# Kernel optimization log

Hardware: AMD Instinct MI355X
Metric: run time of the kernel (lower is better)

The kernel has to match this reference:

```python
import jax, jax.numpy as jnp
import numpy as np


def setup_inputs() -> dict:
    key = jax.random.key(0)
    ks = jax.random.split(key, 7)
    B, IN, H = 4096, 2048, 2048
    initrange = 1.0 / np.sqrt(H)
    return {
        "x": jax.random.normal(ks[0], (B, IN), dtype=jnp.float32),
        "h_prev": jax.random.normal(ks[1], (B, H), dtype=jnp.float32),
        "c_prev": jax.random.normal(ks[2], (B, H), dtype=jnp.float32),
        "W_x": jax.random.uniform(ks[3], (4 * H, IN), minval=-initrange, maxval=initrange, dtype=jnp.float32),
        "b_x": jax.random.uniform(ks[4], (4 * H,), minval=-initrange, maxval=initrange, dtype=jnp.float32),
        "W_h": jax.random.uniform(ks[5], (4 * H, H), minval=-initrange, maxval=initrange, dtype=jnp.float32),
        "b_h": jax.random.uniform(ks[6], (4 * H,), minval=-initrange, maxval=initrange, dtype=jnp.float32),
    }


def reference(x, h_prev, c_prev, W_x, b_x, W_h, b_h):
    # gates = Linear_x(x) + Linear_h(h_prev), shape [B, 4H]
    gates = x @ W_x.T + b_x + h_prev @ W_h.T + b_h
    i, f, g, o = jnp.split(gates, 4, axis=1)  # chunk order in original: i, f, g, o
    i = jax.nn.sigmoid(i)
    f = jax.nn.sigmoid(f)
    g = jnp.tanh(g)
    o = jax.nn.sigmoid(o)
    c = f * c_prev + i * g
    h = o * jnp.tanh(c)
    return (h, c)
```

## Files before the change

### kernel.cpp

```cpp
#include <hip/hip_runtime.h>
#include <hip/hip_bf16.h>
#include <stdint.h>


#define M_DIM 4096
#define N_PACK 8192
#define K_DIM 4096
#define H_DIM 2048

typedef __attribute__((ext_vector_type(8))) short bf16x8;
typedef __attribute__((ext_vector_type(4))) float f32x4;
typedef __attribute__((ext_vector_type(8))) unsigned short ushortx8;

__device__ __forceinline__ unsigned short f2bf(float f) {
    union { float f; uint32_t u; } v; v.f = f;
    uint32_t u = v.u;
    uint32_t r = (u + 0x7FFFu + ((u >> 16) & 1u)) >> 16;
    return (unsigned short)r;
}

__device__ __forceinline__ float fsigmoid(float x) { return 1.0f / (1.0f + __expf(-x)); }
__device__ __forceinline__ float ftanh(float x) { return 2.0f * fsigmoid(2.0f * x) - 1.0f; }

__global__ __launch_bounds__(256) void pack_a(const float* __restrict__ x,
                                              const float* __restrict__ h,
                                              unsigned short* __restrict__ A) {
    int i = blockIdx.x * 256 + threadIdx.x;
    int e = i * 8;
    int row = e >> 12;
    int col = e & 4095;
    const float* src = (col < H_DIM) ? (x + (size_t)row * H_DIM + col)
                                     : (h + (size_t)row * H_DIM + (col - H_DIM));
    float4 f0 = ((const float4*)src)[0];
    float4 f1 = ((const float4*)src)[1];
    ushortx8 o;
    o[0] = f2bf(f0.x); o[1] = f2bf(f0.y); o[2] = f2bf(f0.z); o[3] = f2bf(f0.w);
    o[4] = f2bf(f1.x); o[5] = f2bf(f1.y); o[6] = f2bf(f1.z); o[7] = f2bf(f1.w);
    *(ushortx8*)(A + e) = o;
}

__global__ __launch_bounds__(256) void pack_w(const float* __restrict__ Wx,
                                              const float* __restrict__ Wh,
                                              unsigned short* __restrict__ W) {
    int i = blockIdx.x * 256 + threadIdx.x;
    int e = i * 8;
    int p = e >> 12;
    int k = e & 4095;
    int g  = (p >> 4) & 3;
    int j  = ((p >> 6) << 4) | (p & 15);
    int orig = g * H_DIM + j;
    const float* src = (k < H_DIM) ? (Wx + (size_t)orig * H_DIM + k)
                                   : (Wh + (size_t)orig * H_DIM + (k - H_DIM));
    float4 f0 = ((const float4*)src)[0];
    float4 f1 = ((const float4*)src)[1];
    ushortx8 o;
    o[0] = f2bf(f0.x); o[1] = f2bf(f0.y); o[2] = f2bf(f0.z); o[3] = f2bf(f0.w);
    o[4] = f2bf(f1.x); o[5] = f2bf(f1.y); o[6] = f2bf(f1.z); o[7] = f2bf(f1.w);
    *(ushortx8*)(W + (size_t)p * K_DIM + k) = o;
}

__device__ __forceinline__ void gload_lds16(const void* g, void* l) {
    __builtin_amdgcn_global_load_lds(
        (const __attribute__((address_space(1))) void*)g,
        (__attribute__((address_space(3))) void*)l, 16, 0, 0);
}

#define BAR() __builtin_amdgcn_s_barrier()
#define LGKM0() asm volatile("s_waitcnt lgkmcnt(0)" ::: "memory")
#define VMCNT2() asm volatile("s_waitcnt vmcnt(2)" ::: "memory")
#define VMCNT0() asm volatile("s_waitcnt vmcnt(0)" ::: "memory")

__global__ __launch_bounds__(512, 2) void lstm_gemm8(
        const unsigned short* __restrict__ A,
        const unsigned short* __restrict__ W,
        const float* __restrict__ bx, const float* __restrict__ bh,
        const float* __restrict__ c_prev, float* __restrict__ out) {
    __shared__ char lds[2][2][32768];

    const int tid  = threadIdx.x;
    const int wid  = tid >> 6;
    const int lane = tid & 63;
    const int wr   = wid >> 2;
    const int wc   = wid & 3;

    const int swz = (blockIdx.x & 7) * 64 + (blockIdx.x >> 3);
    const int bm  = swz & 15;
    const int bn  = swz >> 4;

    const char* Ab = (const char*)A + (size_t)(bm * 256) * (K_DIM * 2);
    const char* Wb = (const char*)W + (size_t)(bn * 256) * (K_DIM * 2);

    const int srow = tid >> 3;
    const int skb  = ((tid & 7) << 4) ^ ((srow & 7) << 4);

    auto stage_half = [&](int buf, int mat, int h, int kt) {
        const char* gb = mat ? Wb : Ab;
        #pragma unroll
        for (int qq = 0; qq < 2; ++qq) {
            int q = h * 2 + qq;
            const char* src = gb + (size_t)(q * 64 + srow) * (K_DIM * 2) + kt * 128 + skb;
            gload_lds16(src, &lds[buf][mat][q * 8192 + tid * 16]);
        }
    };

    f32x4 acc[8][4] = {};
    bf16x8 A0[4][2], A1[4][2], Bq[2][2];

    auto read_a = [&](int buf, int qm, bf16x8 (&ar)[4][2]) {
        #pragma unroll
        for (int mf = 0; mf < 4; ++mf) {
            int row = wr * 128 + (qm * 4 + mf) * 16 + (lane & 15);
            #pragma unroll
            for (int kk = 0; kk < 2; ++kk) {
                int cb = (kk * 64 + ((lane >> 4) << 4)) ^ ((row & 7) << 4);
                ar[mf][kk] = *(const bf16x8*)&lds[buf][0][row * 128 + cb];
            }
        }
    };
    auto read_b = [&](int buf, int qn) {
        #pragma unroll
        for (int nf = 0; nf < 2; ++nf) {
            int row = wc * 64 + (qn * 2 + nf) * 16 + (lane & 15);
            #pragma unroll
            for (int kk = 0; kk < 2; ++kk) {
                int cb = (kk * 64 + ((lane >> 4) << 4)) ^ ((row & 7) << 4);
                Bq[nf][kk] = *(const bf16x8*)&lds[buf][1][row * 128 + cb];
            }
        }
    };

#define MMA_Q(QM, QN, AR)                                                      \
    do {                                                                       \
        __builtin_amdgcn_s_setprio(1);                                         \
        _Pragma("unroll")                                                      \
        for (int mf = 0; mf < 4; ++mf) {                                       \
            _Pragma("unroll")                                                  \
            for (int nf = 0; nf < 2; ++nf) {                                   \
                _Pragma("unroll")                                              \
                for (int kk = 0; kk < 2; ++kk) {                               \
                    acc[(QM)*4+mf][(QN)*2+nf] =                                \
                        __builtin_amdgcn_mfma_f32_16x16x32_bf16(               \
                            AR[mf][kk], Bq[nf][kk],                            \
                            acc[(QM)*4+mf][(QN)*2+nf], 0, 0, 0);               \
                }                                                              \
            }                                                                  \
        }                                                                      \
        __builtin_amdgcn_s_setprio(0);                                         \
    } while (0)

    stage_half(0, 0, 0, 0); stage_half(0, 0, 1, 0);
    stage_half(0, 1, 0, 0); stage_half(0, 1, 1, 0);
    stage_half(1, 0, 0, 1);
    VMCNT2();
    BAR();

    for (int it = 0; it < 32; ++it) {
        const int t1   = 2 * it + 1;
        const bool last = (it == 31);

        read_a(0, 0, A0); read_b(0, 0);
        stage_half(1, 0, 1, t1);
        BAR(); LGKM0(); MMA_Q(0, 0, A0); BAR();

        read_a(0, 1, A1);
        stage_half(1, 1, 0, t1);
        BAR(); LGKM0(); MMA_Q(1, 0, A1); BAR();

        read_b(0, 1);
        stage_half(1, 1, 1, t1);
        BAR(); LGKM0(); MMA_Q(0, 1, A0); BAR();

        if (!last) { stage_half(0, 0, 0, t1 + 1); VMCNT2(); }
        else       { VMCNT0(); }
        BAR(); LGKM0(); MMA_Q(1, 1, A1); BAR();

        read_a(1, 0, A0); read_b(1, 0);
        if (!last) stage_half(0, 0, 1, t1 + 1);
        BAR(); LGKM0(); MMA_Q(0, 0, A0); BAR();

        read_a(1, 1, A1);
        if (!last) stage_half(0, 1, 0, t1 + 1);
        BAR(); LGKM0(); MMA_Q(1, 0, A1); BAR();

        read_b(1, 1);
        if (!last) stage_half(0, 1, 1, t1 + 1);
        BAR(); LGKM0(); MMA_Q(0, 1, A0); BAR();

        if (!last) { stage_half(1, 0, 0, t1 + 2); VMCNT2(); }
        else       { VMCNT0(); }
        BAR(); LGKM0(); MMA_Q(1, 1, A1); BAR();
    }

    const int jlo  = lane & 15;
    const int rgrp = lane >> 4;
    const int j    = (bn * 4 + wc) * 16 + jlo;

    const float bi  = bx[j]             + bh[j];
    const float bff = bx[H_DIM + j]     + bh[H_DIM + j];
    const float bg  = bx[2 * H_DIM + j] + bh[2 * H_DIM + j];
    const float bo  = bx[3 * H_DIM + j] + bh[3 * H_DIM + j];

    float* out_h = out;
    float* out_c = out + (size_t)M_DIM * H_DIM;

    #pragma unroll
    for (int m = 0; m < 8; ++m) {
        int row0 = bm * 256 + wr * 128 + m * 16 + rgrp * 4;
        #pragma unroll
        for (int r = 0; r < 4; ++r) {
            int row = row0 + r;
            float pi = acc[m][0][r] + bi;
            float pf = acc[m][1][r] + bff;
            float pg = acc[m][2][r] + bg;
            float po = acc[m][3][r] + bo;
            float i_ = fsigmoid(pi);
            float f_ = fsigmoid(pf);
            float g_ = ftanh(pg);
            float o_ = fsigmoid(po);
            float cp = c_prev[(size_t)row * H_DIM + j];
            float c  = f_ * cp + i_ * g_;
            float hh = o_ * ftanh(c);
            out_h[(size_t)row * H_DIM + j] = hh;
            out_c[(size_t)row * H_DIM + j] = c;
        }
    }
}

extern "C" void kernel_launch(void* const* d_in, const int* in_sizes, int n_in,
                              void* d_out, int out_size, void* d_ws, size_t ws_size,
                              hipStream_t stream) {
    const float* x      = (const float*)d_in[0];
    const float* h_prev = (const float*)d_in[1];
    const float* c_prev = (const float*)d_in[2];
    const float* Wx     = (const float*)d_in[3];
    const float* bx     = (const float*)d_in[4];
    const float* Wh     = (const float*)d_in[5];
    const float* bh     = (const float*)d_in[6];

    unsigned short* Acat = (unsigned short*)d_ws;
    unsigned short* Wp   = (unsigned short*)d_ws + (size_t)M_DIM * K_DIM;

    float* out = (float*)d_out;

    pack_a<<<8192, 256, 0, stream>>>(x, h_prev, Acat);
    pack_w<<<16384, 256, 0, stream>>>(Wx, Wh, Wp);
    lstm_gemm8<<<512, 512, 0, stream>>>(Acat, Wp, bx, bh, c_prev, out);
}
```

Before: 474.8 us.

## Restructure double-buffered prefetch to stage whole matrices later in each half-iteration

Replaces the half-matrix staging spread across all eight MMA phases with whole-matrix loads issued in the last two phases of each half-iteration. The wait drops from vmcnt(2) to vmcnt(8), and the now-redundant lgkmcnt waits before the final MMA of each half are removed. The intent is to issue fewer, larger load batches and to cut waits and barrier stalls. In exchange, prefetches are issued later, which leaves less time to hide global latency and may leave the load and compute phases unevenly balanced.

```diff
diff --git a/kernel.cpp b/kernel.cpp
--- a/kernel.cpp
+++ b/kernel.cpp
@@ -67,7 +67,7 @@
 
 #define BAR() __builtin_amdgcn_s_barrier()
 #define LGKM0() asm volatile("s_waitcnt lgkmcnt(0)" ::: "memory")
-#define VMCNT2() asm volatile("s_waitcnt vmcnt(2)" ::: "memory")
+#define VMCNT8() asm volatile("s_waitcnt vmcnt(8)" ::: "memory")
 #define VMCNT0() asm volatile("s_waitcnt vmcnt(0)" ::: "memory")
 
 __global__ __launch_bounds__(512, 2) void lstm_gemm8(
@@ -93,11 +93,10 @@
     const int srow = tid >> 3;
     const int skb  = ((tid & 7) << 4) ^ ((srow & 7) << 4);
 
-    auto stage_half = [&](int buf, int mat, int h, int kt) {
+    auto stage_mat = [&](int buf, int mat, int kt) {
         const char* gb = mat ? Wb : Ab;
         #pragma unroll
-        for (int qq = 0; qq < 2; ++qq) {
-            int q = h * 2 + qq;
+        for (int q = 0; q < 4; ++q) {
             const char* src = gb + (size_t)(q * 64 + srow) * (K_DIM * 2) + kt * 128 + skb;
             gload_lds16(src, &lds[buf][mat][q * 8192 + tid * 16]);
         }
@@ -148,47 +147,42 @@
         __builtin_amdgcn_s_setprio(0);                                         \
     } while (0)
 
-    stage_half(0, 0, 0, 0); stage_half(0, 0, 1, 0);
-    stage_half(0, 1, 0, 0); stage_half(0, 1, 1, 0);
-    stage_half(1, 0, 0, 1);
-    VMCNT2();
+    stage_mat(0, 0, 0); stage_mat(0, 1, 0);
+    stage_mat(1, 0, 1); stage_mat(1, 1, 1);
+    VMCNT8();
     BAR();
 
     for (int it = 0; it < 32; ++it) {
-        const int t1   = 2 * it + 1;
+        const int te2  = 2 * it + 2;
+        const int to2  = 2 * it + 3;
         const bool last = (it == 31);
 
         read_a(0, 0, A0); read_b(0, 0);
-        stage_half(1, 0, 1, t1);
         BAR(); LGKM0(); MMA_Q(0, 0, A0); BAR();
 
         read_a(0, 1, A1);
-        stage_half(1, 1, 0, t1);
         BAR(); LGKM0(); MMA_Q(1, 0, A1); BAR();
 
         read_b(0, 1);
-        stage_half(1, 1, 1, t1);
+        if (!last) stage_mat(0, 0, te2);
         BAR(); LGKM0(); MMA_Q(0, 1, A0); BAR();
 
-        if (!last) { stage_half(0, 0, 0, t1 + 1); VMCNT2(); }
+        if (!last) { stage_mat(0, 1, te2); VMCNT8(); }
         else       { VMCNT0(); }
-        BAR(); LGKM0(); MMA_Q(1, 1, A1); BAR();
+        BAR(); MMA_Q(1, 1, A1); BAR();
 
         read_a(1, 0, A0); read_b(1, 0);
-        if (!last) stage_half(0, 0, 1, t1 + 1);
         BAR(); LGKM0(); MMA_Q(0, 0, A0); BAR();
 
         read_a(1, 1, A1);
-        if (!last) stage_half(0, 1, 0, t1 + 1);
         BAR(); LGKM0(); MMA_Q(1, 0, A1); BAR();
 
         read_b(1, 1);
-        if (!last) stage_half(0, 1, 1, t1 + 1);
+        if (!last) stage_mat(1, 0, to2);
         BAR(); LGKM0(); MMA_Q(0, 1, A0); BAR();
 
-        if (!last) { stage_half(1, 0, 0, t1 + 2); VMCNT2(); }
-        else       { VMCNT0(); }
-        BAR(); LGKM0(); MMA_Q(1, 1, A1); BAR();
+        if (!last) { stage_mat(1, 1, to2); VMCNT8(); }
+        BAR(); MMA_Q(1, 1, A1); BAR();
     }
 
     const int jlo  = lane & 15;
```

Measured after the change: 477.9 us. About the same (+0.6%).
